# Kernel tuning notes

Hardware: AMD Instinct MI355X
Metric: run time of the kernel (lower is better)

Reference implementation:

```python
import jax, jax.numpy as jnp
import numpy as np

N = 8192  # n_nodes
E = 262144  # edges per adjacency (avg degree 32)


def setup_inputs() -> dict:
    key = jax.random.key(0)
    k0, k1, k2, k3, k4, k5 = jax.random.split(key, 6)
    rows_s = jax.random.randint(k0, (E,), 0, N)
    cols_s = jax.random.randint(k1, (E,), 0, N)
    vals_s = jax.random.uniform(k2, (E,), dtype=jnp.float32)
    rows_t = jax.random.randint(k3, (E,), 0, N)
    cols_t = jax.random.randint(k4, (E,), 0, N)
    vals_t = jax.random.uniform(k5, (E,), dtype=jnp.float32)
    gamma = jnp.zeros((1,), dtype=jnp.float32)  # learnable scalar, init 0.0
    return {
        "rows_s": rows_s, "cols_s": cols_s, "vals_s": vals_s,
        "rows_t": rows_t, "cols_t": cols_t, "vals_t": vals_t,
        "gamma": gamma,
    }


def reference(rows_s, cols_s, vals_s, rows_t, cols_t, vals_t, gamma):
    # coalesce + to_dense: scatter-add duplicates into dense [N, N]
    As = jnp.zeros((N, N), dtype=vals_s.dtype).at[rows_s, cols_s].add(vals_s)
    At = jnp.zeros((N, N), dtype=vals_t.dtype).at[rows_t, cols_t].add(vals_t)
    alpha = jax.nn.sigmoid(gamma[0])
    Af = alpha * As + (1.0 - alpha) * At
    row_sum = jnp.sum(Af, axis=1, keepdims=True)  # [N, 1]
    row_sum = jnp.where(row_sum == 0, jnp.ones_like(row_sum), row_sum)
    Af = Af / row_sum
    # torch returns Af.to_sparse(); dense Af is the equivalent value-complete output
    return Af
```

## Files before the change

### kernel.cpp

```cpp
#include <hip/hip_runtime.h>
#include <math.h>

#define NN 8192
#define NE 262144
#define TOTAL (2*NE)
#define CAP 128
#define CSTR 16
#define HALF 4096

typedef float f4 __attribute__((ext_vector_type(4)));

struct Pair { int c; float v; };

#define CNT_BYTES ((size_t)NN * CSTR * 4)
#define BK_OFF ((size_t)1 << 20)
#define OV_OFF (BK_OFF + (size_t)NN * CAP * sizeof(Pair))

__global__ __launch_bounds__(256) void fill_kernel(
        const int* __restrict__ rows_s, const int* __restrict__ cols_s,
        const float* __restrict__ vals_s,
        const int* __restrict__ rows_t, const int* __restrict__ cols_t,
        const float* __restrict__ vals_t,
        const float* __restrict__ gamma,
        int* __restrict__ cnt, Pair* __restrict__ bucket,
        int* __restrict__ ovf_cnt, int4* __restrict__ ovf) {
    int i = blockIdx.x * blockDim.x + threadIdx.x;
    float alpha = 1.0f / (1.0f + expf(-gamma[0]));
    int r, c; float v, w;
    if (i < NE) { r = rows_s[i]; c = cols_s[i]; v = vals_s[i]; w = alpha; }
    else { int j = i - NE; r = rows_t[j]; c = cols_t[j]; v = vals_t[j]; w = 1.0f - alpha; }
    float wv = w * v;
    int pos = atomicAdd(&cnt[r * CSTR], 1);
    if (pos < CAP) {
        Pair p; p.c = c; p.v = wv;
        bucket[r * CAP + pos] = p;
    } else {
        int k = atomicAdd(ovf_cnt, 1);
        int4 e; e.x = r; e.y = c; e.z = __float_as_int(wv); e.w = 0;
        ovf[k] = e;
    }
}

__global__ __launch_bounds__(256) void row_kernel(
        const int* __restrict__ cnt, const Pair* __restrict__ bucket,
        const int* __restrict__ ovf_cnt, const int4* __restrict__ ovf,
        float* __restrict__ out) {
    __shared__ float row[HALF];
    __shared__ float red[4];
    int b = blockIdx.x;
    int r = b >> 1;
    int base = (b & 1) << 12;
    int t = threadIdx.x;

    f4* row4 = (f4*)row;
    #pragma unroll
    for (int k = t; k < HALF / 4; k += 256) {
        f4 z = {0.f, 0.f, 0.f, 0.f};
        row4[k] = z;
    }
    int n = cnt[r * CSTR];
    int nb = n < CAP ? n : CAP;
    __syncthreads();

    float part = 0.0f;
    for (int k = t; k < nb; k += 256) {
        Pair p = bucket[r * CAP + k];
        part += p.v;
        int cl = p.c - base;
        if ((unsigned)cl < HALF) atomicAdd(&row[cl], p.v);
    }
    int no = *ovf_cnt;
    if (no > 0) {
        for (int k = t; k < no; k += 256) {
            int4 e = ovf[k];
            if (e.x == r) {
                float v = __int_as_float(e.z);
                part += v;
                int cl = e.y - base;
                if ((unsigned)cl < HALF) atomicAdd(&row[cl], v);
            }
        }
    }

    #pragma unroll
    for (int o = 32; o > 0; o >>= 1) part += __shfl_down(part, o, 64);
    if ((t & 63) == 0) red[t >> 6] = part;
    __syncthreads();
    float total = red[0] + red[1] + red[2] + red[3];
    float inv = (total == 0.0f) ? 1.0f : 1.0f / total;

    f4* out4 = (f4*)(out + (size_t)r * NN + base);
    #pragma unroll
    for (int k = t; k < HALF / 4; k += 256) {
        f4 x = row4[k];
        x *= inv;
        __builtin_nontemporal_store(x, &out4[k]);
    }
}

extern "C" void kernel_launch(void* const* d_in, const int* in_sizes, int n_in,
                              void* d_out, int out_size, void* d_ws, size_t ws_size,
                              hipStream_t stream) {
    const int*   rows_s = (const int*)  d_in[0];
    const int*   cols_s = (const int*)  d_in[1];
    const float* vals_s = (const float*)d_in[2];
    const int*   rows_t = (const int*)  d_in[3];
    const int*   cols_t = (const int*)  d_in[4];
    const float* vals_t = (const float*)d_in[5];
    const float* gamma  = (const float*)d_in[6];

    float* out     = (float*)d_out;
    char*  ws      = (char*)d_ws;
    int*   cnt     = (int*)ws;
    int*   ovf_cnt = (int*)(ws + CNT_BYTES);
    Pair*  bucket  = (Pair*)(ws + BK_OFF);
    int4*  ovf     = (int4*)(ws + OV_OFF);

    (void)hipMemsetAsync(ws, 0, CNT_BYTES + 4, stream);

    fill_kernel<<<TOTAL / 256, 256, 0, stream>>>(rows_s, cols_s, vals_s,
                                                 rows_t, cols_t, vals_t,
                                                 gamma, cnt, bucket, ovf_cnt, ovf);
    row_kernel<<<2 * NN, 256, 0, stream>>>(cnt, bucket, ovf_cnt, ovf, out);
}
```

Baseline: 313.7 us.

## Fuse fill and row-normalize kernels into one cooperative kernel with grid sync

Merges the bucket-fill kernel and the per-row densify/normalize kernel into a single cooperative launch. A grid-wide sync separates the two phases, and each of the 2048 blocks then processes 8 half-rows in turn. The per-row counters are packed densely instead of padded to 16 ints, which shrinks the memset. This removes one kernel launch and boundary, but it needs all 2048 blocks to be resident at once and pays for a grid barrier. Dense counters also increase atomic contention on shared cache lines.

```diff
diff --git a/kernel.cpp b/kernel.cpp
--- a/kernel.cpp
+++ b/kernel.cpp
@@ -1,100 +1,104 @@
 #include <hip/hip_runtime.h>
+#include <hip/hip_cooperative_groups.h>
 #include <math.h>
 
 #define NN 8192
 #define NE 262144
 #define TOTAL (2*NE)
 #define CAP 128
-#define CSTR 16
 #define HALF 4096
 
 typedef float f4 __attribute__((ext_vector_type(4)));
 
 struct Pair { int c; float v; };
 
-#define CNT_BYTES ((size_t)NN * CSTR * 4)
-#define BK_OFF ((size_t)1 << 20)
+#define BK_OFF 65536
 #define OV_OFF (BK_OFF + (size_t)NN * CAP * sizeof(Pair))
 
-__global__ __launch_bounds__(256) void fill_kernel(
+__global__ __launch_bounds__(256, 8) void fused_kernel(
         const int* __restrict__ rows_s, const int* __restrict__ cols_s,
         const float* __restrict__ vals_s,
         const int* __restrict__ rows_t, const int* __restrict__ cols_t,
         const float* __restrict__ vals_t,
         const float* __restrict__ gamma,
         int* __restrict__ cnt, Pair* __restrict__ bucket,
-        int* __restrict__ ovf_cnt, int4* __restrict__ ovf) {
-    int i = blockIdx.x * blockDim.x + threadIdx.x;
-    float alpha = 1.0f / (1.0f + expf(-gamma[0]));
-    int r, c; float v, w;
-    if (i < NE) { r = rows_s[i]; c = cols_s[i]; v = vals_s[i]; w = alpha; }
-    else { int j = i - NE; r = rows_t[j]; c = cols_t[j]; v = vals_t[j]; w = 1.0f - alpha; }
-    float wv = w * v;
-    int pos = atomicAdd(&cnt[r * CSTR], 1);
-    if (pos < CAP) {
-        Pair p; p.c = c; p.v = wv;
-        bucket[r * CAP + pos] = p;
-    } else {
-        int k = atomicAdd(ovf_cnt, 1);
-        int4 e; e.x = r; e.y = c; e.z = __float_as_int(wv); e.w = 0;
-        ovf[k] = e;
-    }
-}
-
-__global__ __launch_bounds__(256) void row_kernel(
-        const int* __restrict__ cnt, const Pair* __restrict__ bucket,
-        const int* __restrict__ ovf_cnt, const int4* __restrict__ ovf,
+        int* __restrict__ ovf_cnt, int4* __restrict__ ovf,
         float* __restrict__ out) {
     __shared__ float row[HALF];
     __shared__ float red[4];
-    int b = blockIdx.x;
-    int r = b >> 1;
-    int base = (b & 1) << 12;
+    int i = blockIdx.x * blockDim.x + threadIdx.x;
     int t = threadIdx.x;
 
-    f4* row4 = (f4*)row;
-    #pragma unroll
-    for (int k = t; k < HALF / 4; k += 256) {
-        f4 z = {0.f, 0.f, 0.f, 0.f};
-        row4[k] = z;
-    }
-    int n = cnt[r * CSTR];
-    int nb = n < CAP ? n : CAP;
-    __syncthreads();
-
-    float part = 0.0f;
-    for (int k = t; k < nb; k += 256) {
-        Pair p = bucket[r * CAP + k];
-        part += p.v;
-        int cl = p.c - base;
-        if ((unsigned)cl < HALF) atomicAdd(&row[cl], p.v);
-    }
-    int no = *ovf_cnt;
-    if (no > 0) {
-        for (int k = t; k < no; k += 256) {
-            int4 e = ovf[k];
-            if (e.x == r) {
-                float v = __int_as_float(e.z);
-                part += v;
-                int cl = e.y - base;
-                if ((unsigned)cl < HALF) atomicAdd(&row[cl], v);
-            }
+    float alpha = 1.0f / (1.0f + expf(-gamma[0]));
+    {
+        int r, c; float v, w;
+        if (i < NE) { r = rows_s[i]; c = cols_s[i]; v = vals_s[i]; w = alpha; }
+        else { int j = i - NE; r = rows_t[j]; c = cols_t[j]; v = vals_t[j]; w = 1.0f - alpha; }
+        float wv = w * v;
+        int pos = atomicAdd(&cnt[r], 1);
+        if (pos < CAP) {
+            Pair p; p.c = c; p.v = wv;
+            bucket[r * CAP + pos] = p;
+        } else {
+            int k = atomicAdd(ovf_cnt, 1);
+            int4 e; e.x = r; e.y = c; e.z = __float_as_int(wv); e.w = 0;
+            ovf[k] = e;
         }
     }
 
-    #pragma unroll
-    for (int o = 32; o > 0; o >>= 1) part += __shfl_down(part, o, 64);
-    if ((t & 63) == 0) red[t >> 6] = part;
-    __syncthreads();
-    float total = red[0] + red[1] + red[2] + red[3];
-    float inv = (total == 0.0f) ? 1.0f : 1.0f / total;
+    __threadfence();
+    cooperative_groups::this_grid().sync();
 
-    f4* out4 = (f4*)(out + (size_t)r * NN + base);
-    #pragma unroll
-    for (int k = t; k < HALF / 4; k += 256) {
-        f4 x = row4[k];
-        x *= inv;
-        __builtin_nontemporal_store(x, &out4[k]);
+    int no = *ovf_cnt;
+    for (int step = 0; step < 8; ++step) {
+        int hb = blockIdx.x * 8 + step;
+        int r = hb >> 1;
+        int base = (hb & 1) << 12;
+
+        f4* row4 = (f4*)row;
+        #pragma unroll
+        for (int k = t; k < HALF / 4; k += 256) {
+            f4 z = {0.f, 0.f, 0.f, 0.f};
+            row4[k] = z;
+        }
+        int n = cnt[r];
+        int nb = n < CAP ? n : CAP;
+        __syncthreads();
+
+        float part = 0.0f;
+        for (int k = t; k < nb; k += 256) {
+            Pair p = bucket[r * CAP + k];
+            part += p.v;
+            int cl = p.c - base;
+            if ((unsigned)cl < HALF) atomicAdd(&row[cl], p.v);
+        }
+        if (no > 0) {
+            for (int k = t; k < no; k += 256) {
+                int4 e = ovf[k];
+                if (e.x == r) {
+                    float v = __int_as_float(e.z);
+                    part += v;
+                    int cl = e.y - base;
+                    if ((unsigned)cl < HALF) atomicAdd(&row[cl], v);
+                }
+            }
+        }
+
+        #pragma unroll
+        for (int o = 32; o > 0; o >>= 1) part += __shfl_down(part, o, 64);
+        if ((t & 63) == 0) red[t >> 6] = part;
+        __syncthreads();
+        float total = red[0] + red[1] + red[2] + red[3];
+        float inv = (total == 0.0f) ? 1.0f : 1.0f / total;
+
+        f4* out4 = (f4*)(out + (size_t)r * NN + base);
+        #pragma unroll
+        for (int k = t; k < HALF / 4; k += 256) {
+            f4 x = row4[k];
+            x *= inv;
+            __builtin_nontemporal_store(x, &out4[k]);
+        }
+        __syncthreads();
     }
 }
 
@@ -112,14 +116,15 @@
     float* out     = (float*)d_out;
     char*  ws      = (char*)d_ws;
     int*   cnt     = (int*)ws;
-    int*   ovf_cnt = (int*)(ws + CNT_BYTES);
+    int*   ovf_cnt = (int*)(ws + 32768);
     Pair*  bucket  = (Pair*)(ws + BK_OFF);
     int4*  ovf     = (int4*)(ws + OV_OFF);
 
-    (void)hipMemsetAsync(ws, 0, CNT_BYTES + 4, stream);
+    (void)hipMemsetAsync(ws, 0, 32772, stream);
 
-    fill_kernel<<<TOTAL / 256, 256, 0, stream>>>(rows_s, cols_s, vals_s,
-                                                 rows_t, cols_t, vals_t,
-                                                 gamma, cnt, bucket, ovf_cnt, ovf);
-    row_kernel<<<2 * NN, 256, 0, stream>>>(cnt, bucket, ovf_cnt, ovf, out);
+    void* args[] = { &rows_s, &cols_s, &vals_s, &rows_t, &cols_t, &vals_t,
+                     &gamma, &cnt, &bucket, &ovf_cnt, &ovf, &out };
+    (void)hipLaunchCooperativeKernel((const void*)fused_kernel,
+                                     dim3(TOTAL / 256), dim3(256),
+                                     args, 0, stream);
 }
```

Result: slower. 706.3 us (+125.1%).
